# Optimization experiments

Measured on AMD Instinct MI355X. Metric: run time of the kernel, lower is better.

Reference implementation:

```python
import jax, jax.numpy as jnp
import numpy as np

MAX_SEQ, D, VOCAB, N_LAYERS = 2048, 256, 240, 6
DH = 64.0  # scale used inside RelativeGlobalAttention
BATCH = 4


def _pos_embedding():
    # sin(pow(pos*1e-5, i/D) - pi/2 * ((i+1)%2)), exactly as in __init__
    pos = np.arange(MAX_SEQ, dtype=np.float64)[:, None]
    i = np.arange(D, dtype=np.float64)[None, :]
    ang = np.power(pos * 1e-5, i / D) - np.pi * 0.5 * ((i + 1) % 2)
    return jnp.asarray(np.sin(ang), dtype=jnp.float32)  # [L, D]


def _skew(QE):
    # pad a zero column in front, reshape [B,L,L+1]->[B,L+1,L], drop first row
    B, L, _ = QE.shape
    cat = jnp.concatenate([jnp.zeros((B, L, 1), QE.dtype), QE], axis=2)
    return cat.reshape(B, L + 1, L)[:, 1:, :]


def _rel_attn(x, Wq, Wk, Wv):
    Q = x @ Wq  # [B,L,D]
    K = x @ Wk
    V = x @ Wv
    QE = jnp.einsum('bld,bmd->blm', Q, K - Q)      # Q @ (K-Q)^T
    Srel = _skew(QE)
    QKt = jnp.einsum('bld,bmd->blm', Q, K)
    scores = (QKt + Srel) / jnp.sqrt(jnp.asarray(DH, x.dtype))
    probs = jax.nn.softmax(scores, axis=-1)        # no causal mask in source
    return probs @ V


def setup_inputs() -> dict:
    key = jax.random.key(0)
    ks = jax.random.split(key, 16)
    s = 1.0 / np.sqrt(D)
    mk = lambda k, shape, sc: (jax.random.normal(k, shape, jnp.float32) * sc)
    inp = {
        'tokens': jax.random.randint(ks[0], (BATCH, MAX_SEQ), 0, VOCAB),
        'embed_table': mk(ks[1], (VOCAB, D), 0.05),
        'Wq1': mk(ks[2], (N_LAYERS, D, D), s),
        'Wk1': mk(ks[3], (N_LAYERS, D, D), s),
        'Wv1': mk(ks[4], (N_LAYERS, D, D), s),
        'Wq2': mk(ks[5], (N_LAYERS, D, D), s),
        'Wk2': mk(ks[6], (N_LAYERS, D, D), s),
        'Wv2': mk(ks[7], (N_LAYERS, D, D), s),
        'Wf1': mk(ks[8], (N_LAYERS, D, D), s),
        'bf1': jnp.zeros((N_LAYERS, D), jnp.float32),
        'Wf2': mk(ks[9], (N_LAYERS, D, D), s),
        'bf2': jnp.zeros((N_LAYERS, D), jnp.float32),
        'Wfc': mk(ks[10], (MAX_SEQ * D, VOCAB), 1.0 / np.sqrt(MAX_SEQ * D)),
        'bfc': jnp.zeros((VOCAB,), jnp.float32),
    }
    return inp


def reference(tokens, embed_table, Wq1, Wk1, Wv1, Wq2, Wk2, Wv2,
              Wf1, bf1, Wf2, bf2, Wfc, bfc):
    x = embed_table[tokens] + _pos_embedding()[None]  # [B,L,D]
    for i in range(N_LAYERS):
        x = _rel_attn(x, Wq1[i], Wk1[i], Wv1[i]) + x
        x = _rel_attn(x, Wq2[i], Wk2[i], Wv2[i]) + x
        h = jax.nn.leaky_relu(x @ Wf1[i] + bf1[i], negative_slope=0.2)
        x = h @ Wf2[i] + bf2[i]
        # NOTE: BatchNorm layers exist in source but are never called in _decoder
    flat = x.reshape(x.shape[0], -1)  # [B, L*D]
    return jax.nn.softmax(flat @ Wfc + bfc, axis=-1)  # [B, vocab]
```

## Files before the change

### kernel.cpp

```cpp
#include <hip/hip_runtime.h>
#include <hip/hip_fp16.h>

typedef unsigned short u16;
typedef unsigned int   u32;

#define BB 4
#define LL 2048
#define DD 256
#define VV 240
#define NLAYERS 6

static constexpr long BLD = (long)BB * LL * DD;
static constexpr long LD_ = (long)LL * DD;
static constexpr long LxL = (long)LL * LL;
static constexpr long BLL = (long)BB * LxL;

typedef _Float16 h8  __attribute__((ext_vector_type(8)));
typedef float  f32x4 __attribute__((ext_vector_type(4)));

__device__ __forceinline__ u16 f2h(float f) {
    _Float16 h = (_Float16)f;
    return __builtin_bit_cast(u16, h);
}
__device__ __forceinline__ float h2f(u16 u) {
    return (float)__builtin_bit_cast(_Float16, u);
}

__device__ __forceinline__ void gl16(const void* g, void* l) {
    __builtin_amdgcn_global_load_lds((const __attribute__((address_space(1))) void*)g,
                                     (__attribute__((address_space(3))) void*)l, 16, 0, 0);
}

__device__ __forceinline__ uint3 swz_bid() {
    const int gx = gridDim.x, gy = gridDim.y;
    const int nwg = gx * gy * gridDim.z;
    const int lin = blockIdx.x + gx * (blockIdx.y + gy * blockIdx.z);
    const int q = nwg >> 3;
    const int swz = (lin & 7) * q + (lin >> 3);
    uint3 r;
    r.x = swz % gx;
    const int t2 = swz / gx;
    r.y = t2 % gy;
    r.z = t2 / gy;
    return r;
}

__global__ __launch_bounds__(256)
void embed_kernel(const int* __restrict__ tokens, const float* __restrict__ table,
                  float* __restrict__ x, u16* __restrict__ xh)
{
    long idx = (long)blockIdx.x * 256 + threadIdx.x;
    if (idx >= BLD) return;
    int i  = (int)(idx & (DD - 1));
    long bl = idx >> 8;
    int l  = (int)(bl & (LL - 1));
    int tok = tokens[bl];
    float base = (float)l * 1e-5f;
    float p = powf(base, (float)i * (1.0f / (float)DD));
    float ang = p - ((i & 1) ? 0.0f : 1.57079632679489662f);
    float v = table[(long)tok * DD + i] + sinf(ang);
    x[idx] = v;
    xh[idx] = f2h(v);
}

template<bool DIFF>
__global__ __launch_bounds__(256)
void wconv(const float* __restrict__ W, const float* __restrict__ Wsub,
           u16* __restrict__ Wt, long lstride)
{
    int blk = blockIdx.x;
    int m  = blk >> 6;
    int ti = (blk >> 3) & 7;
    int tj = blk & 7;
    const float* src = W + (long)m * 65536;
    u16* dst = Wt + (long)m * lstride;
    __shared__ float tile[32][33];
    int t = threadIdx.x;
    int c = t & 31, r8 = t >> 5;
    #pragma unroll
    for (int p = 0; p < 4; ++p) {
        int r = r8 + p * 8;
        long off = (long)(ti * 32 + r) * 256 + tj * 32 + c;
        float v = src[off];
        if constexpr (DIFF) v -= Wsub[(long)m * 65536 + off];
        tile[r][c] = v;
    }
    __syncthreads();
    #pragma unroll
    for (int p = 0; p < 4; ++p) {
        int n = r8 + p * 8;
        dst[(long)(tj * 32 + n) * 256 + ti * 32 + c] = f2h(tile[c][n]);
    }
}

template<int EPI, int BM, int BN>
__global__ __launch_bounds__(256)
void gemm_mfma(const u16* __restrict__ A, const u16* __restrict__ B,
               const u16* __restrict__ B2,
               const float* __restrict__ bias, const float* __restrict__ Cres,
               float* __restrict__ Cf, u16* __restrict__ Ch,
               u16* __restrict__ Ch2, u16* __restrict__ Ch3, u16* __restrict__ Ch4,
               int M, int N, int K, int ldA,
               long sA, long sB, long sC)
{
    constexpr int FM = BM / 32, FN = BN / 32;
    __shared__ u16 As[2][BM * 32];
    __shared__ u16 Bs[2][BN * 32];
    const uint3 bid = swz_bid();
    const int bz = bid.z;
    A += (long)bz * sA;
    const int bm = bid.y * BM;
    const int bn = bid.x * BN;
    int bnb = bn;
    const u16* Bp;
    if constexpr (EPI & 128) {
        Bp = (bn >= LL) ? B2 : B;
        if (bn >= LL) bnb = bn - LL;
        Bp += (long)bz * sB;
    } else {
        Bp = B + (long)bz * sB;
    }
    if constexpr (EPI & 4)  Cres += (long)bz * sC;
    if constexpr (EPI & 8)  Cf   += (long)bz * sC;
    if constexpr ((EPI & 16) && !(EPI & (64 | 128))) Ch += (long)bz * sC;

    const int t = threadIdx.x;
    const int lane = t & 63, wave = t >> 6;
    const int wm = (wave >> 1) * (BM / 2), wn = (wave & 1) * (BN / 2);

    f32x4 acc[FM][FN];
    #pragma unroll
    for (int i = 0; i < FM; ++i)
        #pragma unroll
        for (int j = 0; j < FN; ++j)
            acc[i][j] = (f32x4){0.f, 0.f, 0.f, 0.f};

    const u16* gA0 = A  + (long)(bm  + (t >> 2)) * ldA + (t & 3) * 8;
    const u16* gB0 = Bp + (long)(bnb + (t >> 2)) * K   + (t & 3) * 8;

    const int arow = wm + (lane & 15);
    const int brow = wn + (lane & 15);
    const int ko = (lane >> 4) * 8;

    #define STAGE(buf, koff) do {                                              \
        gl16(gA0 + (koff), &As[buf][wave * 512]);                              \
        if constexpr (BM == 128) gl16(gA0 + 64L * ldA + (koff),                \
                                      &As[buf][2048 + wave * 512]);            \
        gl16(gB0 + (koff), &Bs[buf][wave * 512]);                              \
        if constexpr (BN == 128) gl16(gB0 + 64L * K + (koff),                  \
                                      &Bs[buf][2048 + wave * 512]);            \
    } while (0)

    STAGE(0, 0);
    int cur = 0;
    for (int k0 = 0; k0 < K; k0 += 32) {
        __syncthreads();
        if (k0 + 32 < K) {
            if (cur) STAGE(0, k0 + 32);
            else     STAGE(1, k0 + 32);
        }
        h8 af[FM], bf[FN];
        #pragma unroll
        for (int i = 0; i < FM; ++i) af[i] = *(const h8*)&As[cur][(arow + i * 16) * 32 + ko];
        #pragma unroll
        for (int j = 0; j < FN; ++j) bf[j] = *(const h8*)&Bs[cur][(brow + j * 16) * 32 + ko];
        #pragma unroll
        for (int i = 0; i < FM; ++i)
            #pragma unroll
            for (int j = 0; j < FN; ++j)
                acc[i][j] = __builtin_amdgcn_mfma_f32_16x16x32_f16(af[i], bf[j], acc[i][j], 0, 0, 0);
        cur ^= 1;
    }
    #undef STAGE

    const int colc = lane & 15;
    const int rowb = (lane >> 4) * 4;
    if constexpr (EPI & 64) {
        const int seg = bn >> 8;
        const int nb  = bn & 255;
        if (seg < 3) {
            u16* dst = (seg == 0) ? Ch : ((seg == 1) ? Ch2 : Ch3);
            #pragma unroll
            for (int i = 0; i < FM; ++i)
                #pragma unroll
                for (int j = 0; j < FN; ++j) {
                    int nn = nb + wn + j * 16 + colc;
                    #pragma unroll
                    for (int r = 0; r < 4; ++r) {
                        long row = bm + wm + i * 16 + rowb + r;
                        dst[row * DD + nn] = f2h(acc[i][j][r]);
                    }
                }
        } else {
            #pragma unroll
            for (int i = 0; i < FM; ++i) {
                int r0 = bm + wm + i * 16 + rowb;
                int b  = r0 >> 11;
                int m0 = r0 & (LL - 1);
                #pragma unroll
                for (int j = 0; j < FN; ++j) {
                    int nn = nb + wn + j * 16 + colc;
                    f32x4 v = acc[i][j];
                    ushort4 pk;
                    pk.x = f2h(v.x); pk.y = f2h(v.y); pk.z = f2h(v.z); pk.w = f2h(v.w);
                    *(ushort4*)&Ch4[((long)b * DD + nn) * LL + m0] = pk;
                }
            }
        }
    } else if constexpr (EPI & 128) {
        u16* dst = ((bn >= LL) ? Ch2 : Ch) + (long)bz * sC;
        const int nb = bn & (LL - 1);
        #pragma unroll
        for (int i = 0; i < FM; ++i)
            #pragma unroll
            for (int j = 0; j < FN; ++j) {
                int n = nb + wn + j * 16 + colc;
                #pragma unroll
                for (int r = 0; r < 4; ++r) {
                    long row = bm + wm + i * 16 + rowb + r;
                    dst[row * LL + n] = f2h(acc[i][j][r]);
                }
            }
    } else {
        #pragma unroll
        for (int i = 0; i < FM; ++i) {
            #pragma unroll
            for (int j = 0; j < FN; ++j) {
                int n = bn + wn + j * 16 + colc;
                float bv = (EPI & 1) ? bias[n] : 0.f;
                #pragma unroll
                for (int r = 0; r < 4; ++r) {
                    long row = bm + wm + i * 16 + rowb + r;
                    float val = acc[i][j][r] + bv;
                    if (EPI & 2) val = (val >= 0.f) ? val : 0.2f * val;
                    long off = row * (long)N + n;
                    if (EPI & 4) val += Cres[off];
                    if (EPI & 8) Cf[off] = val;
                    if (EPI & 16) Ch[off] = f2h(val);
                }
            }
        }
    }
}

__global__ __launch_bounds__(256)
void skew_softmax(u16* __restrict__ S1, const u16* __restrict__ QE)
{
    const int bi = blockIdx.x;
    const int b = bi >> 11;
    const int i = bi & (LL - 1);
    u16* srow = S1 + (long)bi * LL;
    const u16* qe_i  = QE + ((long)b * LL + i) * LL;
    const u16* qe_i1 = qe_i + ((i + 1 < LL) ? LL : 0);
    const int t = threadIdx.x;

    uint4 sv = ((const uint4*)srow)[t];
    const u16* se = (const u16*)&sv;
    float vals[8];
    float mx = -1e30f;
    #pragma unroll
    for (int j = 0; j < 8; ++j) {
        int m = t * 8 + j;
        float srel;
        if (m <= i)            srel = h2f(qe_i[m - i + (LL - 1)]);
        else if (m == i + 1)   srel = 0.f;
        else                   srel = h2f(qe_i1[m - i - 2]);
        float s = (h2f(se[j]) + srel) * 0.125f;
        vals[j] = s;
        mx = fmaxf(mx, s);
    }
    #pragma unroll
    for (int off = 32; off >= 1; off >>= 1)
        mx = fmaxf(mx, __shfl_xor(mx, off, 64));
    __shared__ float redm[4], reds[4];
    const int wid = t >> 6;
    if ((t & 63) == 0) redm[wid] = mx;
    __syncthreads();
    mx = fmaxf(fmaxf(redm[0], redm[1]), fmaxf(redm[2], redm[3]));

    float sum = 0.f;
    #pragma unroll
    for (int j = 0; j < 8; ++j) { vals[j] = expf(vals[j] - mx); sum += vals[j]; }
    #pragma unroll
    for (int off = 32; off >= 1; off >>= 1)
        sum += __shfl_xor(sum, off, 64);
    if ((t & 63) == 0) reds[wid] = sum;
    __syncthreads();
    sum = reds[0] + reds[1] + reds[2] + reds[3];
    float inv = 1.0f / sum;
    uint4 ov;
    u16* oe = (u16*)&ov;
    #pragma unroll
    for (int j = 0; j < 8; ++j) oe[j] = f2h(vals[j] * inv);
    ((uint4*)srow)[t] = ov;
}

__global__ __launch_bounds__(960)
void fc_partial(const float* __restrict__ x, const float* __restrict__ W,
                float* __restrict__ part)
{
    const int v = threadIdx.x;
    const int b = threadIdx.y;
    const int chunk = blockIdx.x;
    const int KC = (int)(LD_ / 256);
    const long k0 = (long)chunk * KC;
    const float* xb = x + (long)b * LD_ + k0;
    const float* Wp = W + k0 * VV + v;
    float acc = 0.f;
    #pragma unroll 4
    for (int k2 = 0; k2 < KC; ++k2)
        acc = fmaf(xb[k2], Wp[(long)k2 * VV], acc);
    part[((long)chunk * BB + b) * VV + v] = acc;
}

__global__ __launch_bounds__(960)
void fc_finish(const float* __restrict__ part, const float* __restrict__ bias,
               float* __restrict__ out)
{
    const int v = threadIdx.x, b = threadIdx.y;
    float acc = bias[v];
    for (int c = 0; c < 256; ++c)
        acc += part[((long)c * BB + b) * VV + v];
    __shared__ float lds[BB][VV];
    __shared__ float mxs[BB], sms[BB];
    lds[b][v] = acc;
    __syncthreads();
    if (v == 0) {
        float m = -1e30f;
        for (int j = 0; j < VV; ++j) m = fmaxf(m, lds[b][j]);
        float s = 0.f;
        for (int j = 0; j < VV; ++j) s += expf(lds[b][j] - m);
        mxs[b] = m; sms[b] = s;
    }
    __syncthreads();
    out[b * VV + v] = expf(lds[b][v] - mxs[b]) / sms[b];
}

extern "C" void kernel_launch(void* const* d_in, const int* in_sizes, int n_in,
                              void* d_out, int out_size, void* d_ws, size_t ws_size,
                              hipStream_t stream)
{
    const int*   tokens = (const int*)d_in[0];
    const float* table  = (const float*)d_in[1];
    const float* Wq1 = (const float*)d_in[2];
    const float* Wk1 = (const float*)d_in[3];
    const float* Wv1 = (const float*)d_in[4];
    const float* Wq2 = (const float*)d_in[5];
    const float* Wk2 = (const float*)d_in[6];
    const float* Wv2 = (const float*)d_in[7];
    const float* Wf1 = (const float*)d_in[8];
    const float* bf1 = (const float*)d_in[9];
    const float* Wf2 = (const float*)d_in[10];
    const float* bf2 = (const float*)d_in[11];
    const float* Wfc = (const float*)d_in[12];
    const float* bfc = (const float*)d_in[13];

    char* p = (char*)d_ws;
    float* x  = (float*)p; p += BLD * 4;
    u16* xh = (u16*)p;     p += BLD * 2;
    u16* qb = (u16*)p;     p += BLD * 2;
    u16* kb = (u16*)p;     p += BLD * 2;
    u16* eb = (u16*)p;     p += BLD * 2;
    u16* vt = (u16*)p;     p += BLD * 2;
    u16* S1 = (u16*)p;     p += BLL * 2;
    u16* QE = (u16*)p;     p += BLL * 2;
    u16* qkevw = (u16*)p;  p += 12L * 4 * 65536 * 2;
    u16* fw = (u16*)p;     p += 12L * 65536 * 2;
    float* part = (float*)p;
    u16* hb = qb;

    const long LS = 4 * 65536;
    wconv<false><<<384, 256, 0, stream>>>(Wq1, nullptr, qkevw + 0L * 65536, LS);
    wconv<false><<<384, 256, 0, stream>>>(Wk1, nullptr, qkevw + 1L * 65536, LS);
    wconv<true ><<<384, 256, 0, stream>>>(Wk1, Wq1,     qkevw + 2L * 65536, LS);
    wconv<false><<<384, 256, 0, stream>>>(Wv1, nullptr, qkevw + 3L * 65536, LS);
    wconv<false><<<384, 256, 0, stream>>>(Wq2, nullptr, qkevw + 24L * 65536, LS);
    wconv<true ><<<384, 256, 0, stream>>>(Wk2, Wq2,     qkevw + 24L * 65536 + 2 * 65536, LS);
    wconv<false><<<384, 256, 0, stream>>>(Wk2, nullptr, qkevw + 24L * 65536 + 1 * 65536, LS);
    wconv<false><<<384, 256, 0, stream>>>(Wv2, nullptr, qkevw + 24L * 65536 + 3 * 65536, LS);
    wconv<false><<<384, 256, 0, stream>>>(Wf1, nullptr, fw, 65536);
    wconv<false><<<384, 256, 0, stream>>>(Wf2, nullptr, fw + 6L * 65536, 65536);

    embed_kernel<<<(int)((BLD + 255) / 256), 256, 0, stream>>>(tokens, table, x, xh);

    const dim3 gqkev(8, 64, 1);
    const dim3 gscore(32, 16, BB);
    const dim3 gpv(4, 16, BB);
    const dim3 gffn(4, 64, 1);

    for (int layer = 0; layer < NLAYERS; ++layer) {
        for (int half = 0; half < 2; ++half) {
            const u16* wqkev = qkevw + ((long)(half * 6 + layer)) * LS;
            gemm_mfma<64, 128, 128><<<gqkev, 256, 0, stream>>>(
                xh, wqkev, nullptr, nullptr, nullptr, nullptr, qb, kb, eb, vt,
                BB * LL, 1024, DD, DD, 0, 0, 0);
            gemm_mfma<128, 128, 128><<<gscore, 256, 0, stream>>>(
                qb, kb, eb, nullptr, nullptr, nullptr, S1, QE, nullptr, nullptr,
                LL, LL, DD, DD, LD_, LD_, LxL);
            skew_softmax<<<BB * LL, 256, 0, stream>>>(S1, QE);
            gemm_mfma<4 | 8 | 16, 128, 64><<<gpv, 256, 0, stream>>>(
                S1, vt, nullptr, nullptr, x, x, xh, nullptr, nullptr, nullptr,
                LL, DD, LL, LL, LxL, LD_, LD_);
        }
        gemm_mfma<1 | 2 | 16, 128, 64><<<gffn, 256, 0, stream>>>(
            xh, fw + (long)layer * 65536, nullptr, bf1 + layer * DD, nullptr,
            nullptr, hb, nullptr, nullptr, nullptr, BB * LL, DD, DD, DD, 0, 0, 0);
        gemm_mfma<1 | 8 | 16, 128, 64><<<gffn, 256, 0, stream>>>(
            hb, fw + (long)(6 + layer) * 65536, nullptr, bf2 + layer * DD, nullptr,
            x, xh, nullptr, nullptr, nullptr, BB * LL, DD, DD, DD, 0, 0, 0);
    }

    fc_partial<<<256, dim3(VV, BB, 1), 0, stream>>>(x, Wfc, part);
    fc_finish<<<1, dim3(VV, BB, 1), 0, stream>>>(part, bfc, (float*)d_out);
}
```

Baseline: 1.665 ms.

## Triple-buffer GEMM LDS staging with vmcnt waits and swap grid block mapping

Moves the MFMA GEMM from double to triple-buffered LDS staging, issuing loads two k-steps ahead. It replaces the full __syncthreads with an explicit s_waitcnt vmcnt plus s_barrier, so later loads can stay in flight while the current tile is computed. It also adds a template flag that swaps which grid axis maps to M and N, and reorders the launch grids, which changes the order in which tiles are walked under the workgroup swizzle. The cost is more LDS per block, which may lower occupancy. The hand-written vmcnt counts must match the number of loads each STAGE issues per thread, or LDS data could be read before it arrives.

```diff
diff --git a/kernel.cpp b/kernel.cpp
--- a/kernel.cpp
+++ b/kernel.cpp
@@ -29,6 +29,13 @@
 __device__ __forceinline__ void gl16(const void* g, void* l) {
     __builtin_amdgcn_global_load_lds((const __attribute__((address_space(1))) void*)g,
                                      (__attribute__((address_space(3))) void*)l, 16, 0, 0);
+}
+
+template<int N> __device__ __forceinline__ void waitvm() {
+    if constexpr (N == 0) asm volatile("s_waitcnt vmcnt(0)" ::: "memory");
+    else if constexpr (N == 3) asm volatile("s_waitcnt vmcnt(3)" ::: "memory");
+    else if constexpr (N == 4) asm volatile("s_waitcnt vmcnt(4)" ::: "memory");
+    else                      asm volatile("s_waitcnt vmcnt(0)" ::: "memory");
 }
 
 __device__ __forceinline__ uint3 swz_bid() {
@@ -93,7 +100,7 @@
     }
 }
 
-template<int EPI, int BM, int BN>
+template<int EPI, int BM, int BN, bool SW>
 __global__ __launch_bounds__(256)
 void gemm_mfma(const u16* __restrict__ A, const u16* __restrict__ B,
                const u16* __restrict__ B2,
@@ -104,13 +111,15 @@
                long sA, long sB, long sC)
 {
     constexpr int FM = BM / 32, FN = BN / 32;
-    __shared__ u16 As[2][BM * 32];
-    __shared__ u16 Bs[2][BN * 32];
+    constexpr int LPS = ((BM == 128) ? 2 : 1) + ((BN == 128) ? 2 : 1);
+    __shared__ u16 As[3][BM * 32];
+    __shared__ u16 Bs[3][BN * 32];
+
     const uint3 bid = swz_bid();
     const int bz = bid.z;
     A += (long)bz * sA;
-    const int bm = bid.y * BM;
-    const int bn = bid.x * BN;
+    const int bm = (SW ? bid.x : bid.y) * BM;
+    const int bn = (SW ? bid.y : bid.x) * BN;
     int bnb = bn;
     const u16* Bp;
     if constexpr (EPI & 128) {
@@ -152,24 +161,28 @@
     } while (0)
 
     STAGE(0, 0);
+    if (32 < K) STAGE(1, 32);
     int cur = 0;
     for (int k0 = 0; k0 < K; k0 += 32) {
-        __syncthreads();
-        if (k0 + 32 < K) {
-            if (cur) STAGE(0, k0 + 32);
-            else     STAGE(1, k0 + 32);
-        }
+        if (k0 + 32 < K) waitvm<LPS>();
+        else             waitvm<0>();
+        __builtin_amdgcn_s_barrier();
+        __builtin_amdgcn_sched_barrier(0);
+        if (k0 + 64 < K)
+            STAGE((cur + 2) % 3, k0 + 64);
         h8 af[FM], bf[FN];
         #pragma unroll
-        for (int i = 0; i < FM; ++i) af[i] = *(const h8*)&As[cur][(arow + i * 16) * 32 + ko];
-        #pragma unroll
-        for (int j = 0; j < FN; ++j) bf[j] = *(const h8*)&Bs[cur][(brow + j * 16) * 32 + ko];
+        for (int i = 0; i < FM; ++i)
+            af[i] = *(const h8*)&As[cur][(arow + i * 16) * 32 + ko];
+        #pragma unroll
+        for (int j = 0; j < FN; ++j)
+            bf[j] = *(const h8*)&Bs[cur][(brow + j * 16) * 32 + ko];
         #pragma unroll
         for (int i = 0; i < FM; ++i)
             #pragma unroll
             for (int j = 0; j < FN; ++j)
                 acc[i][j] = __builtin_amdgcn_mfma_f32_16x16x32_f16(af[i], bf[j], acc[i][j], 0, 0, 0);
-        cur ^= 1;
+        cur = (cur + 1) % 3;
     }
     #undef STAGE
 
@@ -383,29 +396,29 @@
 
     embed_kernel<<<(int)((BLD + 255) / 256), 256, 0, stream>>>(tokens, table, x, xh);
 
-    const dim3 gqkev(8, 64, 1);
+    const dim3 gqkev(64, 8, 1);
     const dim3 gscore(32, 16, BB);
-    const dim3 gpv(4, 16, BB);
-    const dim3 gffn(4, 64, 1);
+    const dim3 gpv(16, 4, BB);
+    const dim3 gffn(64, 4, 1);
 
     for (int layer = 0; layer < NLAYERS; ++layer) {
         for (int half = 0; half < 2; ++half) {
             const u16* wqkev = qkevw + ((long)(half * 6 + layer)) * LS;
-            gemm_mfma<64, 128, 128><<<gqkev, 256, 0, stream>>>(
+            gemm_mfma<64, 128, 128, true><<<gqkev, 256, 0, stream>>>(
                 xh, wqkev, nullptr, nullptr, nullptr, nullptr, qb, kb, eb, vt,
                 BB * LL, 1024, DD, DD, 0, 0, 0);
-            gemm_mfma<128, 128, 128><<<gscore, 256, 0, stream>>>(
+            gemm_mfma<128, 128, 128, false><<<gscore, 256, 0, stream>>>(
                 qb, kb, eb, nullptr, nullptr, nullptr, S1, QE, nullptr, nullptr,
                 LL, LL, DD, DD, LD_, LD_, LxL);
             skew_softmax<<<BB * LL, 256, 0, stream>>>(S1, QE);
-            gemm_mfma<4 | 8 | 16, 128, 64><<<gpv, 256, 0, stream>>>(
+            gemm_mfma<4 | 8 | 16, 128, 64, true><<<gpv, 256, 0, stream>>>(
                 S1, vt, nullptr, nullptr, x, x, xh, nullptr, nullptr, nullptr,
                 LL, DD, LL, LL, LxL, LD_, LD_);
         }
-        gemm_mfma<1 | 2 | 16, 128, 64><<<gffn, 256, 0, stream>>>(
+        gemm_mfma<1 | 2 | 16, 128, 64, true><<<gffn, 256, 0, stream>>>(
             xh, fw + (long)layer * 65536, nullptr, bf1 + layer * DD, nullptr,
             nullptr, hb, nullptr, nullptr, nullptr, BB * LL, DD, DD, DD, 0, 0, 0);
-        gemm_mfma<1 | 8 | 16, 128, 64><<<gffn, 256, 0, stream>>>(
+        gemm_mfma<1 | 8 | 16, 128, 64, true><<<gffn, 256, 0, stream>>>(
             hb, fw + (long)(6 + layer) * 65536, nullptr, bf2 + layer * DD, nullptr,
             x, xh, nullptr, nullptr, nullptr, BB * LL, DD, DD, DD, 0, 0, 0);
     }
```

Result: slower. 1.832 ms (+10.0%).

## Compute QK^T and Q(K-Q)^T in one dual-output kernel sharing Q tiles

Applied to the files above, without the earlier changes.

Replaces the score GEMM, which ran over a doubled N dimension covering the K and E=(K-Q) operands, with a 512-thread kernel. Each block loads one Q tile once, and two wave groups multiply it against the K tile and the E tile, writing S1 and QE. This halves the Q tile loads and the block count for the score stage, at the cost of more LDS per block and possibly lower occupancy. It also merges the ten weight-conversion launches into a single kernel driven by a pointer table.

```diff
diff --git a/kernel.cpp b/kernel.cpp
--- a/kernel.cpp
+++ b/kernel.cpp
@@ -63,17 +63,25 @@
     xh[idx] = f2h(v);
 }
 
-template<bool DIFF>
+struct WcArgs {
+    const float* src[10];
+    const float* sub[10];
+    u16*         dst[10];
+    long         lstride[10];
+};
+
 __global__ __launch_bounds__(256)
-void wconv(const float* __restrict__ W, const float* __restrict__ Wsub,
-           u16* __restrict__ Wt, long lstride)
+void wconv_all(WcArgs a)
 {
     int blk = blockIdx.x;
-    int m  = blk >> 6;
-    int ti = (blk >> 3) & 7;
-    int tj = blk & 7;
-    const float* src = W + (long)m * 65536;
-    u16* dst = Wt + (long)m * lstride;
+    int which = blk / 384;
+    int rest  = blk % 384;
+    int m  = rest >> 6;
+    int ti = (rest >> 3) & 7;
+    int tj = rest & 7;
+    const float* src = a.src[which] + (long)m * 65536;
+    const float* sub = a.sub[which];
+    u16* dst = a.dst[which] + (long)m * a.lstride[which];
     __shared__ float tile[32][33];
     int t = threadIdx.x;
     int c = t & 31, r8 = t >> 5;
@@ -82,7 +90,7 @@
         int r = r8 + p * 8;
         long off = (long)(ti * 32 + r) * 256 + tj * 32 + c;
         float v = src[off];
-        if constexpr (DIFF) v -= Wsub[(long)m * 65536 + off];
+        if (sub) v -= sub[(long)m * 65536 + off];
         tile[r][c] = v;
     }
     __syncthreads();
@@ -96,7 +104,6 @@
 template<int EPI, int BM, int BN>
 __global__ __launch_bounds__(256)
 void gemm_mfma(const u16* __restrict__ A, const u16* __restrict__ B,
-               const u16* __restrict__ B2,
                const float* __restrict__ bias, const float* __restrict__ Cres,
                float* __restrict__ Cf, u16* __restrict__ Ch,
                u16* __restrict__ Ch2, u16* __restrict__ Ch3, u16* __restrict__ Ch4,
@@ -111,18 +118,10 @@
     A += (long)bz * sA;
     const int bm = bid.y * BM;
     const int bn = bid.x * BN;
-    int bnb = bn;
-    const u16* Bp;
-    if constexpr (EPI & 128) {
-        Bp = (bn >= LL) ? B2 : B;
-        if (bn >= LL) bnb = bn - LL;
-        Bp += (long)bz * sB;
-    } else {
-        Bp = B + (long)bz * sB;
-    }
+    const u16* Bp = B + (long)bz * sB;
     if constexpr (EPI & 4)  Cres += (long)bz * sC;
     if constexpr (EPI & 8)  Cf   += (long)bz * sC;
-    if constexpr ((EPI & 16) && !(EPI & (64 | 128))) Ch += (long)bz * sC;
+    if constexpr ((EPI & 16) && !(EPI & 64)) Ch += (long)bz * sC;
 
     const int t = threadIdx.x;
     const int lane = t & 63, wave = t >> 6;
@@ -135,8 +134,8 @@
         for (int j = 0; j < FN; ++j)
             acc[i][j] = (f32x4){0.f, 0.f, 0.f, 0.f};
 
-    const u16* gA0 = A  + (long)(bm  + (t >> 2)) * ldA + (t & 3) * 8;
-    const u16* gB0 = Bp + (long)(bnb + (t >> 2)) * K   + (t & 3) * 8;
+    const u16* gA0 = A  + (long)(bm + (t >> 2)) * ldA + (t & 3) * 8;
+    const u16* gB0 = Bp + (long)(bn + (t >> 2)) * K   + (t & 3) * 8;
 
     const int arow = wm + (lane & 15);
     const int brow = wn + (lane & 15);
@@ -207,20 +206,6 @@
                 }
             }
         }
-    } else if constexpr (EPI & 128) {
-        u16* dst = ((bn >= LL) ? Ch2 : Ch) + (long)bz * sC;
-        const int nb = bn & (LL - 1);
-        #pragma unroll
-        for (int i = 0; i < FM; ++i)
-            #pragma unroll
-            for (int j = 0; j < FN; ++j) {
-                int n = nb + wn + j * 16 + colc;
-                #pragma unroll
-                for (int r = 0; r < 4; ++r) {
-                    long row = bm + wm + i * 16 + rowb + r;
-                    dst[row * LL + n] = f2h(acc[i][j][r]);
-                }
-            }
     } else {
         #pragma unroll
         for (int i = 0; i < FM; ++i) {
@@ -243,6 +228,90 @@
     }
 }
 
+__global__ __launch_bounds__(512)
+void score_dual(const u16* __restrict__ Q, const u16* __restrict__ Kt,
+                const u16* __restrict__ Et,
+                u16* __restrict__ S1, u16* __restrict__ QE)
+{
+    __shared__ u16 As[2][128 * 32];
+    __shared__ u16 Bk[2][128 * 32];
+    __shared__ u16 Be[2][128 * 32];
+    const uint3 bid = swz_bid();
+    const int bz = bid.z;
+    const int bm = bid.y * 128;
+    const int bn = bid.x * 128;
+    const u16* Qb = Q  + (long)bz * LD_;
+    const u16* Kb = Kt + (long)bz * LD_;
+    const u16* Eb = Et + (long)bz * LD_;
+
+    const int t = threadIdx.x;
+    const int lane = t & 63, wave = t >> 6;
+    const int w4 = wave & 3;
+    const int wm = (w4 >> 1) * 64, wn = (w4 & 1) * 64;
+    const bool grpE = wave >= 4;
+
+    f32x4 acc[4][4];
+    #pragma unroll
+    for (int i = 0; i < 4; ++i)
+        #pragma unroll
+        for (int j = 0; j < 4; ++j)
+            acc[i][j] = (f32x4){0.f, 0.f, 0.f, 0.f};
+
+    const int crow = t >> 2, ck = (t & 3) * 8;
+    const u16* gA = Qb + (long)(bm + crow) * DD + ck;
+    const u16* gK = Kb + (long)(bn + crow) * DD + ck;
+    const u16* gE = Eb + (long)(bn + crow) * DD + ck;
+
+    const int arow = wm + (lane & 15);
+    const int brow = wn + (lane & 15);
+    const int ko = (lane >> 4) * 8;
+
+    #define SSTAGE(buf, koff) do {                                             \
+        gl16(gA + (koff), &As[buf][wave * 512]);                               \
+        gl16(gK + (koff), &Bk[buf][wave * 512]);                               \
+        gl16(gE + (koff), &Be[buf][wave * 512]);                               \
+    } while (0)
+
+    SSTAGE(0, 0);
+    int cur = 0;
+    for (int k0 = 0; k0 < DD; k0 += 32) {
+        __syncthreads();
+        if (k0 + 32 < DD) {
+            if (cur) SSTAGE(0, k0 + 32);
+            else     SSTAGE(1, k0 + 32);
+        }
+        const u16* Ab = &As[cur][0];
+        const u16* Bb = grpE ? &Be[cur][0] : &Bk[cur][0];
+        h8 af[4], bf[4];
+        #pragma unroll
+        for (int i = 0; i < 4; ++i) af[i] = *(const h8*)&Ab[(arow + i * 16) * 32 + ko];
+        #pragma unroll
+        for (int j = 0; j < 4; ++j) bf[j] = *(const h8*)&Bb[(brow + j * 16) * 32 + ko];
+        #pragma unroll
+        for (int i = 0; i < 4; ++i)
+            #pragma unroll
+            for (int j = 0; j < 4; ++j)
+                acc[i][j] = __builtin_amdgcn_mfma_f32_16x16x32_f16(af[i], bf[j], acc[i][j], 0, 0, 0);
+        cur ^= 1;
+    }
+    #undef SSTAGE
+
+    const int colc = lane & 15;
+    const int rowb = (lane >> 4) * 4;
+    u16* dst = (grpE ? QE : S1) + (long)bz * LxL;
+    #pragma unroll
+    for (int i = 0; i < 4; ++i)
+        #pragma unroll
+        for (int j = 0; j < 4; ++j) {
+            int n = bn + wn + j * 16 + colc;
+            #pragma unroll
+            for (int r = 0; r < 4; ++r) {
+                long row = bm + wm + i * 16 + rowb + r;
+                dst[row * (long)LL + n] = f2h(acc[i][j][r]);
+            }
+        }
+}
+
 __global__ __launch_bounds__(256)
 void skew_softmax(u16* __restrict__ S1, const u16* __restrict__ QE)
 {
@@ -370,21 +439,23 @@
     u16* hb = qb;
 
     const long LS = 4 * 65536;
-    wconv<false><<<384, 256, 0, stream>>>(Wq1, nullptr, qkevw + 0L * 65536, LS);
-    wconv<false><<<384, 256, 0, stream>>>(Wk1, nullptr, qkevw + 1L * 65536, LS);
-    wconv<true ><<<384, 256, 0, stream>>>(Wk1, Wq1,     qkevw + 2L * 65536, LS);
-    wconv<false><<<384, 256, 0, stream>>>(Wv1, nullptr, qkevw + 3L * 65536, LS);
-    wconv<false><<<384, 256, 0, stream>>>(Wq2, nullptr, qkevw + 24L * 65536, LS);
-    wconv<true ><<<384, 256, 0, stream>>>(Wk2, Wq2,     qkevw + 24L * 65536 + 2 * 65536, LS);
-    wconv<false><<<384, 256, 0, stream>>>(Wk2, nullptr, qkevw + 24L * 65536 + 1 * 65536, LS);
-    wconv<false><<<384, 256, 0, stream>>>(Wv2, nullptr, qkevw + 24L * 65536 + 3 * 65536, LS);
-    wconv<false><<<384, 256, 0, stream>>>(Wf1, nullptr, fw, 65536);
-    wconv<false><<<384, 256, 0, stream>>>(Wf2, nullptr, fw + 6L * 65536, 65536);
+    WcArgs wa;
+    wa.src[0] = Wq1; wa.sub[0] = nullptr; wa.dst[0] = qkevw + 0L * 65536;  wa.lstride[0] = LS;
+    wa.src[1] = Wk1; wa.sub[1] = nullptr; wa.dst[1] = qkevw + 1L * 65536;  wa.lstride[1] = LS;
+    wa.src[2] = Wk1; wa.sub[2] = Wq1;     wa.dst[2] = qkevw + 2L * 65536;  wa.lstride[2] = LS;
+    wa.src[3] = Wv1; wa.sub[3] = nullptr; wa.dst[3] = qkevw + 3L * 65536;  wa.lstride[3] = LS;
+    wa.src[4] = Wq2; wa.sub[4] = nullptr; wa.dst[4] = qkevw + 24L * 65536; wa.lstride[4] = LS;
+    wa.src[5] = Wk2; wa.sub[5] = nullptr; wa.dst[5] = qkevw + 24L * 65536 + 1 * 65536; wa.lstride[5] = LS;
+    wa.src[6] = Wk2; wa.sub[6] = Wq2;     wa.dst[6] = qkevw + 24L * 65536 + 2 * 65536; wa.lstride[6] = LS;
+    wa.src[7] = Wv2; wa.sub[7] = nullptr; wa.dst[7] = qkevw + 24L * 65536 + 3 * 65536; wa.lstride[7] = LS;
+    wa.src[8] = Wf1; wa.sub[8] = nullptr; wa.dst[8] = fw;                  wa.lstride[8] = 65536;
+    wa.src[9] = Wf2; wa.sub[9] = nullptr; wa.dst[9] = fw + 6L * 65536;     wa.lstride[9] = 65536;
+    wconv_all<<<3840, 256, 0, stream>>>(wa);
 
     embed_kernel<<<(int)((BLD + 255) / 256), 256, 0, stream>>>(tokens, table, x, xh);
 
     const dim3 gqkev(8, 64, 1);
-    const dim3 gscore(32, 16, BB);
+    const dim3 gscore(16, 16, BB);
     const dim3 gpv(4, 16, BB);
     const dim3 gffn(4, 64, 1);
 
@@ -392,21 +463,19 @@
         for (int half = 0; half < 2; ++half) {
             const u16* wqkev = qkevw + ((long)(half * 6 + layer)) * LS;
             gemm_mfma<64, 128, 128><<<gqkev, 256, 0, stream>>>(
-                xh, wqkev, nullptr, nullptr, nullptr, nullptr, qb, kb, eb, vt,
+                xh, wqkev, nullptr, nullptr, nullptr, qb, kb, eb, vt,
                 BB * LL, 1024, DD, DD, 0, 0, 0);
-            gemm_mfma<128, 128, 128><<<gscore, 256, 0, stream>>>(
-                qb, kb, eb, nullptr, nullptr, nullptr, S1, QE, nullptr, nullptr,
-                LL, LL, DD, DD, LD_, LD_, LxL);
+            score_dual<<<gscore, 512, 0, stream>>>(qb, kb, eb, S1, QE);
             skew_softmax<<<BB * LL, 256, 0, stream>>>(S1, QE);
             gemm_mfma<4 | 8 | 16, 128, 64><<<gpv, 256, 0, stream>>>(
-                S1, vt, nullptr, nullptr, x, x, xh, nullptr, nullptr, nullptr,
+                S1, vt, nullptr, x, x, xh, nullptr, nullptr, nullptr,
                 LL, DD, LL, LL, LxL, LD_, LD_);
         }
         gemm_mfma<1 | 2 | 16, 128, 64><<<gffn, 256, 0, stream>>>(
-            xh, fw + (long)layer * 65536, nullptr, bf1 + layer * DD, nullptr,
+            xh, fw + (long)layer * 65536, bf1 + layer * DD, nullptr,
             nullptr, hb, nullptr, nullptr, nullptr, BB * LL, DD, DD, DD, 0, 0, 0);
         gemm_mfma<1 | 8 | 16, 128, 64><<<gffn, 256, 0, stream>>>(
-            hb, fw + (long)(6 + layer) * 65536, nullptr, bf2 + layer * DD, nullptr,
+            hb, fw + (long)(6 + layer) * 65536, bf2 + layer * DD, nullptr,
             x, xh, nullptr, nullptr, nullptr, BB * LL, DD, DD, DD, 0, 0, 0);
     }
 
```

Result: no change. 1.695 ms (+1.8%).
